# Kernel tuning notes

Hardware: AMD Instinct MI355X
Metric: run time of the kernel (lower is better)

## Reference

```python
import jax, jax.numpy as jnp
import numpy as np

NUM_MODELS = 64
OUT_F = 256
IN_F = 256
B = 32768
F0 = 2
F1 = 2


def setup_inputs() -> dict:
    key = jax.random.key(0)
    k1, k2, k3, k4 = jax.random.split(key, 4)
    sqrt_k = float(np.sqrt(1.0 / NUM_MODELS))
    weights = 2 * sqrt_k * jax.random.uniform(k1, (NUM_MODELS, OUT_F, IN_F), dtype=jnp.float32) - sqrt_k
    biases = 2 * sqrt_k * jax.random.uniform(k2, (NUM_MODELS, OUT_F), dtype=jnp.float32) - sqrt_k
    inputs = jax.random.normal(k3, (B, IN_F // F1), dtype=jnp.float32)
    indices = jax.random.randint(k4, (B,), 0, NUM_MODELS, dtype=jnp.int64)
    return {"inputs": inputs, "weights": weights, "biases": biases,
            "indices": indices, "factor0": F0, "factor1": F1}


def reference(inputs, weights, biases, indices, factor0, factor1):
    out_sub = weights.shape[1] // factor0
    in_sub = weights.shape[2] // factor1
    # Gather per-sample weight slices: (B, out_sub, in_sub)
    subweight = weights[indices, :out_sub, :in_sub]
    subbias = biases[indices, :out_sub]  # (B, out_sub)
    # Batched matvec + bias
    return jnp.einsum('boi,bi->bo', subweight, inputs) + subbias
```

## Files before the change

kernel.cpp:

```cpp
#include <hip/hip_runtime.h>
#include <hip/hip_bf16.h>

#define NMODELS 64
#define NB      32768
#define INF     256
#define OUTF    256
#define INS     128
#define OUTS    128
#define TILE_M  64
#define NT      10
#define BINCAP  1024
#define NSB     128
#define WCONV_BLOCKS 512

typedef unsigned int u32;
typedef unsigned short u16;
using bf16x8  = __attribute__((ext_vector_type(8))) short;
using f32x4   = __attribute__((ext_vector_type(4))) float;
using float4v = __attribute__((ext_vector_type(4))) float;
using short8v = __attribute__((ext_vector_type(8))) short;

__device__ __forceinline__ u16 f2bf(float f) {
    union { float fv; u32 u; } v; v.fv = f;
    u32 u = v.u;
    u += 0x7fffu + ((u >> 16) & 1u);
    return (u16)(u >> 16);
}

__device__ __forceinline__ void async_copy16(const void* g, void* l) {
    __builtin_amdgcn_global_load_lds((const __attribute__((address_space(1))) u32*)g,
                                     (__attribute__((address_space(3))) u32*)l,
                                     16, 0, 0);
}

__global__ __launch_bounds__(256) void k_scatconv(const int* __restrict__ idx,
                                                  const float* __restrict__ w,
                                                  int* __restrict__ cursors,
                                                  int* __restrict__ perm,
                                                  u16* __restrict__ wb) {
    const int t = threadIdx.x;
    const int b = blockIdx.x;
    if (b < NSB) {
        __shared__ int h[NMODELS];
        __shared__ int base[NMODELS];
        if (t < NMODELS) h[t] = 0;
        __syncthreads();
        const int i = b * 256 + t;
        const int m = idx[i];
        const int r = atomicAdd(&h[m], 1);
        __syncthreads();
        if (t < NMODELS && h[t] != 0) base[t] = atomicAdd(&cursors[t], h[t]);
        __syncthreads();
        perm[(m << 10) + base[m] + r] = i;
    } else {
        const int cid = (b - NSB) * 256 + t;
        const int m   = cid >> 11;
        const int rem = cid & 2047;
        const int row = rem >> 4;
        const int c   = rem & 15;
        const float* src = w + ((size_t)m * OUTF + row) * INF + c * 8;
        float4v v0 = *(const float4v*)(src);
        float4v v1 = *(const float4v*)(src + 4);
        short8v s;
        s[0]=(short)f2bf(v0.x); s[1]=(short)f2bf(v0.y); s[2]=(short)f2bf(v0.z); s[3]=(short)f2bf(v0.w);
        s[4]=(short)f2bf(v1.x); s[5]=(short)f2bf(v1.y); s[6]=(short)f2bf(v1.z); s[7]=(short)f2bf(v1.w);
        *(short8v*)(wb + ((size_t)(m * 128 + row) * 128) + ((c ^ (row & 15)) * 8)) = s;
    }
}

__global__ __launch_bounds__(256) void k_gemm(const float* __restrict__ x,
                                              const u16* __restrict__ wb,
                                              const float* __restrict__ bias,
                                              const int* __restrict__ cursors,
                                              const int* __restrict__ perm,
                                              float* __restrict__ out) {
    __shared__ __align__(16) u16 Ws[OUTS * 128];
    const int m   = blockIdx.x;
    const int cnt = cursors[m];
    if ((int)blockIdx.y * TILE_M >= cnt) return;
    const int t    = threadIdx.x;
    const int wave = t >> 6;
    const int lane = t & 63;
    const int quad = lane >> 4;
    const int lr   = lane & 15;

    {
        const char* g = (const char*)(wb + (size_t)m * (OUTS * 128));
        char* l = (char*)Ws;
        #pragma unroll
        for (int itc = 0; itc < 8; ++itc) {
            const int off = itc * 4096 + wave * 1024;
            async_copy16(g + off + lane * 16, l + off);
        }
    }
    float4v bv4[8];
    #pragma unroll
    for (int nt = 0; nt < 8; ++nt)
        bv4[nt] = *(const float4v*)(bias + m * OUTF + nt * 16 + quad * 4);

    int xoff[4];
    #pragma unroll
    for (int k0 = 0; k0 < 4; ++k0) xoff[k0] = ((k0 * 4 + quad) ^ lr) * 8;
    const int rowbase = lr * 128;
    const int pbase   = m << 10;

    int tile = blockIdx.y;
    int row  = tile * TILE_M + wave * 16 + lr;
    int p    = (row < cnt) ? perm[pbase + row] : -1;
    const float* xr = x + (size_t)((p < 0) ? 0 : p) * INS + quad * 8;
    float4v xa[8];
    #pragma unroll
    for (int k0 = 0; k0 < 4; ++k0) {
        xa[2 * k0]     = *(const float4v*)(xr + k0 * 32);
        xa[2 * k0 + 1] = *(const float4v*)(xr + k0 * 32 + 4);
    }

    __syncthreads();

    for (;;) {
        bf16x8 xb[4];
        #pragma unroll
        for (int k0 = 0; k0 < 4; ++k0) {
            bf16x8 a;
            a[0] = (short)f2bf(xa[2*k0].x);   a[1] = (short)f2bf(xa[2*k0].y);
            a[2] = (short)f2bf(xa[2*k0].z);   a[3] = (short)f2bf(xa[2*k0].w);
            a[4] = (short)f2bf(xa[2*k0+1].x); a[5] = (short)f2bf(xa[2*k0+1].y);
            a[6] = (short)f2bf(xa[2*k0+1].z); a[7] = (short)f2bf(xa[2*k0+1].w);
            xb[k0] = a;
        }
        f32x4 acc[8];
        #pragma unroll
        for (int nt = 0; nt < 8; ++nt) acc[nt] = (f32x4){0.f, 0.f, 0.f, 0.f};
        #pragma unroll
        for (int k0 = 0; k0 < 4; ++k0) {
            #pragma unroll
            for (int nt = 0; nt < 8; ++nt) {
                bf16x8 wfr = *(const bf16x8*)&Ws[nt * 2048 + rowbase + xoff[k0]];
                acc[nt] = __builtin_amdgcn_mfma_f32_16x16x32_bf16(wfr, xb[k0], acc[nt], 0, 0, 0);
            }
        }
        const int curp = p;
        const int ntile = tile + NT;
        const bool more = (ntile * TILE_M < cnt);
        if (more) {
            row = ntile * TILE_M + wave * 16 + lr;
            p   = (row < cnt) ? perm[pbase + row] : -1;
            const float* xr2 = x + (size_t)((p < 0) ? 0 : p) * INS + quad * 8;
            #pragma unroll
            for (int k0 = 0; k0 < 4; ++k0) {
                xa[2 * k0]     = *(const float4v*)(xr2 + k0 * 32);
                xa[2 * k0 + 1] = *(const float4v*)(xr2 + k0 * 32 + 4);
            }
        }
        if (curp >= 0) {
            float* orow = out + (size_t)curp * OUTS + quad * 4;
            #pragma unroll
            for (int nt = 0; nt < 8; ++nt)
                *(float4v*)(orow + nt * 16) = acc[nt] + bv4[nt];
        }
        if (!more) break;
        tile = ntile;
    }
}

extern "C" void kernel_launch(void* const* d_in, const int* in_sizes, int n_in,
                              void* d_out, int out_size, void* d_ws, size_t ws_size,
                              hipStream_t stream) {
    const float* x    = (const float*)d_in[0];
    const float* w    = (const float*)d_in[1];
    const float* bias = (const float*)d_in[2];
    const int*   idx  = (const int*)d_in[3];
    float* out = (float*)d_out;

    int* ws      = (int*)d_ws;
    int* cursors = ws;
    int* perm    = ws + 64;
    u16* wb      = (u16*)(ws + 64 + 65536);

    hipMemsetAsync(cursors, 0, NMODELS * sizeof(int), stream);
    k_scatconv<<<dim3(NSB + WCONV_BLOCKS), dim3(256), 0, stream>>>(idx, w, cursors, perm, wb);
    k_gemm    <<<dim3(NMODELS, NT),        dim3(256), 0, stream>>>(x, wb, bias, cursors, perm, out);
}
```

Before: 94.83 us.

## Replace atomic cursor binning with prefix histogram and split GEMM output halves

Each binning block now recomputes a histogram of all preceding indices in shared memory to obtain deterministic per-model offsets, which removes the global atomic cursors and the memset launch. The last block writes the final per-model counts. The GEMM grid gains a z dimension that splits the 128 output columns into two halves, halving shared weight staging and accumulator registers per block while doubling block count. The trade-off is redundant histogram reads of the index array, up to 32K per block for later blocks, and each x row now being loaded twice across the z blocks.

New measurement: 100.9 us. 1.06x slower.

```diff
diff --git a/kernel.cpp b/kernel.cpp
--- a/kernel.cpp
+++ b/kernel.cpp
@@ -9,7 +9,6 @@
 #define OUTS    128
 #define TILE_M  64
 #define NT      10
-#define BINCAP  1024
 #define NSB     128
 #define WCONV_BLOCKS 512
 
@@ -19,6 +18,7 @@
 using f32x4   = __attribute__((ext_vector_type(4))) float;
 using float4v = __attribute__((ext_vector_type(4))) float;
 using short8v = __attribute__((ext_vector_type(8))) short;
+using int4v   = __attribute__((ext_vector_type(4))) int;
 
 __device__ __forceinline__ u16 f2bf(float f) {
     union { float fv; u32 u; } v; v.fv = f;
@@ -33,25 +33,34 @@
                                      16, 0, 0);
 }
 
-__global__ __launch_bounds__(256) void k_scatconv(const int* __restrict__ idx,
-                                                  const float* __restrict__ w,
-                                                  int* __restrict__ cursors,
-                                                  int* __restrict__ perm,
-                                                  u16* __restrict__ wb) {
+__global__ __launch_bounds__(256) void k_prep(const int* __restrict__ idx,
+                                              const float* __restrict__ w,
+                                              int* __restrict__ counts_g,
+                                              int* __restrict__ perm,
+                                              u16* __restrict__ wb) {
     const int t = threadIdx.x;
     const int b = blockIdx.x;
     if (b < NSB) {
+        __shared__ int hb[NMODELS];
         __shared__ int h[NMODELS];
-        __shared__ int base[NMODELS];
-        if (t < NMODELS) h[t] = 0;
+        if (t < NMODELS) { hb[t] = 0; h[t] = 0; }
         __syncthreads();
-        const int i = b * 256 + t;
+        const int lim = b * 256;
+        for (int c = 0; c * 1024 < lim; ++c) {
+            const int j = c * 1024 + t * 4;
+            if (j < lim) {
+                int4v v = *(const int4v*)(idx + j);
+                atomicAdd(&hb[v.x], 1); atomicAdd(&hb[v.y], 1);
+                atomicAdd(&hb[v.z], 1); atomicAdd(&hb[v.w], 1);
+            }
+        }
+        __syncthreads();
+        const int i = lim + t;
         const int m = idx[i];
         const int r = atomicAdd(&h[m], 1);
+        perm[(m << 10) + hb[m] + r] = i;
         __syncthreads();
-        if (t < NMODELS && h[t] != 0) base[t] = atomicAdd(&cursors[t], h[t]);
-        __syncthreads();
-        perm[(m << 10) + base[m] + r] = i;
+        if (b == NSB - 1 && t < NMODELS) counts_g[t] = hb[t] + h[t];
     } else {
         const int cid = (b - NSB) * 256 + t;
         const int m   = cid >> 11;
@@ -71,13 +80,14 @@
 __global__ __launch_bounds__(256) void k_gemm(const float* __restrict__ x,
                                               const u16* __restrict__ wb,
                                               const float* __restrict__ bias,
-                                              const int* __restrict__ cursors,
+                                              const int* __restrict__ counts_g,
                                               const int* __restrict__ perm,
                                               float* __restrict__ out) {
-    __shared__ __align__(16) u16 Ws[OUTS * 128];
+    __shared__ __align__(16) u16 Ws[64 * 128];
     const int m   = blockIdx.x;
-    const int cnt = cursors[m];
+    const int cnt = counts_g[m];
     if ((int)blockIdx.y * TILE_M >= cnt) return;
+    const int z    = blockIdx.z;
     const int t    = threadIdx.x;
     const int wave = t >> 6;
     const int lane = t & 63;
@@ -85,24 +95,23 @@
     const int lr   = lane & 15;
 
     {
-        const char* g = (const char*)(wb + (size_t)m * (OUTS * 128));
+        const char* g = (const char*)(wb + ((size_t)m * 128 + z * 64) * 128);
         char* l = (char*)Ws;
         #pragma unroll
-        for (int itc = 0; itc < 8; ++itc) {
+        for (int itc = 0; itc < 4; ++itc) {
             const int off = itc * 4096 + wave * 1024;
             async_copy16(g + off + lane * 16, l + off);
         }
     }
-    float4v bv4[8];
+    float4v bv4[4];
     #pragma unroll
-    for (int nt = 0; nt < 8; ++nt)
-        bv4[nt] = *(const float4v*)(bias + m * OUTF + nt * 16 + quad * 4);
+    for (int nt = 0; nt < 4; ++nt)
+        bv4[nt] = *(const float4v*)(bias + m * OUTF + z * 64 + nt * 16 + quad * 4);
 
     int xoff[4];
     #pragma unroll
     for (int k0 = 0; k0 < 4; ++k0) xoff[k0] = ((k0 * 4 + quad) ^ lr) * 8;
-    const int rowbase = lr * 128;
-    const int pbase   = m << 10;
+    const int pbase = m << 10;
 
     int tile = blockIdx.y;
     int row  = tile * TILE_M + wave * 16 + lr;
@@ -128,14 +137,14 @@
             a[6] = (short)f2bf(xa[2*k0+1].z); a[7] = (short)f2bf(xa[2*k0+1].w);
             xb[k0] = a;
         }
-        f32x4 acc[8];
+        f32x4 acc[4];
         #pragma unroll
-        for (int nt = 0; nt < 8; ++nt) acc[nt] = (f32x4){0.f, 0.f, 0.f, 0.f};
+        for (int nt = 0; nt < 4; ++nt) acc[nt] = (f32x4){0.f, 0.f, 0.f, 0.f};
         #pragma unroll
         for (int k0 = 0; k0 < 4; ++k0) {
             #pragma unroll
-            for (int nt = 0; nt < 8; ++nt) {
-                bf16x8 wfr = *(const bf16x8*)&Ws[nt * 2048 + rowbase + xoff[k0]];
+            for (int nt = 0; nt < 4; ++nt) {
+                bf16x8 wfr = *(const bf16x8*)&Ws[(nt * 16 + lr) * 128 + xoff[k0]];
                 acc[nt] = __builtin_amdgcn_mfma_f32_16x16x32_bf16(wfr, xb[k0], acc[nt], 0, 0, 0);
             }
         }
@@ -153,9 +162,9 @@
             }
         }
         if (curp >= 0) {
-            float* orow = out + (size_t)curp * OUTS + quad * 4;
+            float* orow = out + (size_t)curp * OUTS + z * 64 + quad * 4;
             #pragma unroll
-            for (int nt = 0; nt < 8; ++nt)
+            for (int nt = 0; nt < 4; ++nt)
                 *(float4v*)(orow + nt * 16) = acc[nt] + bv4[nt];
         }
         if (!more) break;
@@ -172,12 +181,11 @@
     const int*   idx  = (const int*)d_in[3];
     float* out = (float*)d_out;
 
-    int* ws      = (int*)d_ws;
-    int* cursors = ws;
-    int* perm    = ws + 64;
-    u16* wb      = (u16*)(ws + 64 + 65536);
+    int* ws       = (int*)d_ws;
+    int* counts_g = ws;
+    int* perm     = ws + 64;
+    u16* wb       = (u16*)(ws + 64 + 65536);
 
-    hipMemsetAsync(cursors, 0, NMODELS * sizeof(int), stream);
-    k_scatconv<<<dim3(NSB + WCONV_BLOCKS), dim3(256), 0, stream>>>(idx, w, cursors, perm, wb);
-    k_gemm    <<<dim3(NMODELS, NT),        dim3(256), 0, stream>>>(x, wb, bias, cursors, perm, out);
+    k_prep<<<dim3(NSB + WCONV_BLOCKS), dim3(256), 0, stream>>>(idx, w, counts_g, perm, wb);
+    k_gemm<<<dim3(NMODELS, NT, 2),     dim3(256), 0, stream>>>(x, wb, bias, counts_g, perm, out);
 }
```
